# Kernel tuning notes

Hardware: AMD Instinct MI355X
Metric: run time of the kernel (lower is better)

The kernel has to match this reference:

```python
import jax, jax.numpy as jnp
import numpy as np

N_NODES = 50000
N_EDGES = 800000
D_IN, D_HID, D_ENC = 256, 128, 64


def setup_inputs() -> dict:
    key = jax.random.key(0)
    ks = jax.random.split(key, 8)
    x = jax.random.normal(ks[0], (N_NODES, D_IN), dtype=jnp.float32)
    edge_index = jax.random.randint(ks[1], (2, N_EDGES), 0, N_NODES, dtype=jnp.int64)
    # GCNConv params: lin weight (no bias) + separate bias, stored as [in, out]
    W1 = jax.random.normal(ks[2], (D_IN, D_HID), dtype=jnp.float32) * (1.0 / np.sqrt(D_IN))
    b1 = jnp.zeros((D_HID,), dtype=jnp.float32)
    W2 = jax.random.normal(ks[3], (D_HID, D_ENC), dtype=jnp.float32) * (1.0 / np.sqrt(D_HID))
    b2 = jnp.zeros((D_ENC,), dtype=jnp.float32)
    Wfc = jax.random.normal(ks[4], (D_ENC, 1), dtype=jnp.float32) * (1.0 / np.sqrt(D_ENC))
    bfc = jnp.zeros((1,), dtype=jnp.float32)
    return {"x": x, "edge_index": edge_index, "W1": W1, "b1": b1,
            "W2": W2, "b2": b2, "Wfc": Wfc, "bfc": bfc}


def gcn_conv(x, W, b, row, col, norm, n_nodes):
    """PyG GCNConv (normalize=True): D^-1/2 (A+I) D^-1/2 X W + b."""
    h = x @ W                                   # [N, out]
    msg = h[row] * norm[:, None]                # [E+N, out] gather + scale
    out = jax.ops.segment_sum(msg, col, num_segments=n_nodes)  # scatter-add
    return out + b


def gcn_norm(edge_index, n_nodes, dtype):
    loop = jnp.arange(n_nodes, dtype=edge_index.dtype)
    row = jnp.concatenate([edge_index[0], loop])  # sources
    col = jnp.concatenate([edge_index[1], loop])  # targets
    deg = jax.ops.segment_sum(jnp.ones_like(col, dtype=dtype), col,
                              num_segments=n_nodes)
    dinv = jnp.where(deg > 0, jax.lax.rsqrt(jnp.maximum(deg, 1e-12)), 0.0)
    norm = dinv[row] * dinv[col]
    return row, col, norm


def reference(x, edge_index, W1, b1, W2, b2, Wfc, bfc):
    n = x.shape[0]
    row, col, norm = gcn_norm(edge_index, n, x.dtype)
    h = gcn_conv(x, W1, b1, row, col, norm, n)
    h = jax.nn.relu(h)
    # dropout p=0 / eval mode: identity
    h = gcn_conv(h, W2, b2, row, col, norm, n)
    out = jax.nn.sigmoid(h @ Wfc + bfc)          # [N, 1]
    return out
```

## Files before the change

### kernel.cpp

```cpp
#include <hip/hip_runtime.h>
#include <hip/hip_bf16.h>
#include <cmath>

#define N_NODES 50000
#define N_EDGES 800000
#define D_IN 256
#define D_HID 128
#define D_ENC 64
#define NBUK 128
#define BSH 9
#define BMSK 511
#define BCAP 16384
#define PBF_EPT 8
#define NPARTB 196
#define NGEMB 782
#define NGEMB_H 391
#define GEMM_H2_ROW0 (NGEMB_H * 64)
#define NCSRB 98

typedef short short8 __attribute__((ext_vector_type(8)));
typedef float floatx4 __attribute__((ext_vector_type(4)));
typedef float floatx8 __attribute__((ext_vector_type(8)));
typedef unsigned short ushort8v __attribute__((ext_vector_type(8)));

static __device__ __forceinline__ unsigned short f2bf(float f) {
    unsigned int u = __float_as_uint(f);
    unsigned int r = (u + 0x7FFFu + ((u >> 16) & 1u)) >> 16;
    return (unsigned short)r;
}
static __device__ __forceinline__ float bf2f(unsigned short u) {
    return __uint_as_float(((unsigned int)u) << 16);
}
static __device__ __forceinline__ floatx8 bf2f8(ushort8v u) {
    floatx8 f;
#pragma unroll
    for (int j = 0; j < 8; ++j) f[j] = bf2f(u[j]);
    return f;
}

static __device__ __forceinline__ void wswz(const float* __restrict__ W,
                                            unsigned short* __restrict__ Wsw,
                                            int t, int K, int N) {
    int KS = K / 32;
    int lane = t & 63;
    int ks   = (t >> 6) % KS;
    int ct   = (t >> 6) / KS;
    int m = lane & 15, quad = lane >> 4;
    int kbase = ks * 32 + quad * 8;
    int col   = ct * 16 + m;
#pragma unroll
    for (int j = 0; j < 8; ++j)
        Wsw[t * 8 + j] = f2bf(W[(size_t)(kbase + j) * N + col]);
}

__global__ __launch_bounds__(256) void prep_k(const float* __restrict__ W1,
                                              const float* __restrict__ W2,
                                              const float* __restrict__ b2,
                                              const float* __restrict__ Wfc,
                                              unsigned short* __restrict__ Wsw1,
                                              float* __restrict__ w2fc,
                                              float* __restrict__ b2fc,
                                              int* __restrict__ bcur) {
    int t = blockIdx.x * 256 + threadIdx.x;
    if (t < 4096) wswz(W1, Wsw1, t, D_IN, D_HID);
    else if (t < 4224) {
        int c = t - 4096;
        float s = 0.0f;
#pragma unroll 8
        for (int j = 0; j < D_ENC; ++j) s += W2[c * D_ENC + j] * Wfc[j];
        w2fc[c] = s;
    } else if (t == 4224) {
        float s = 0.0f;
        for (int j = 0; j < D_ENC; ++j) s += b2[j] * Wfc[j];
        b2fc[0] = s;
    } else if (t >= 4225 && t < 4225 + NBUK) {
        bcur[t - 4225] = 0;
    }
}

static __device__ void part_path(char* dynsm, int bid,
                                 const int* __restrict__ rows,
                                 const int* __restrict__ cols,
                                 int* __restrict__ bcur,
                                 unsigned int* __restrict__ brecs) {
    unsigned int* recs = (unsigned int*)dynsm;
    int* h     = (int*)(dynsm + 16384);
    int* ex    = h + NBUK;
    int* gbase = ex + NBUK;
    int tid = threadIdx.x;
    if (tid < NBUK) h[tid] = 0;
    __syncthreads();
    int e0 = bid * 4096;
    unsigned int myrec[PBF_EPT];
    int myb[PBF_EPT];
#pragma unroll
    for (int j = 0; j < PBF_EPT; ++j) {
        int e = e0 + j * 512 + tid;
        if (e < N_EDGES) {
            int s = __builtin_nontemporal_load(&rows[e]);
            int d = __builtin_nontemporal_load(&cols[e]);
            myrec[j] = ((unsigned int)s << 16) | (unsigned int)d;
            myb[j] = d >> BSH;
            atomicAdd(&h[myb[j]], 1);
        } else myb[j] = -1;
    }
    __syncthreads();
    if (tid < NBUK) {
        int c = h[tid];
        gbase[tid] = tid * BCAP + (c ? atomicAdd(&bcur[tid], c) : 0);
        ex[tid] = c;
    }
    __syncthreads();
    for (int off = 1; off < NBUK; off <<= 1) {
        int v = 0;
        if (tid < NBUK && tid >= off) v = ex[tid - off];
        __syncthreads();
        if (tid < NBUK) ex[tid] += v;
        __syncthreads();
    }
    if (tid < NBUK) { ex[tid] -= h[tid]; h[tid] = 0; }
    __syncthreads();
#pragma unroll
    for (int j = 0; j < PBF_EPT; ++j) {
        if (myb[j] >= 0) {
            int p = ex[myb[j]] + atomicAdd(&h[myb[j]], 1);
            recs[p] = myrec[j];
        }
    }
    __syncthreads();
    int w = tid >> 6, lane = tid & 63;
    for (int b = w; b < NBUK; b += 8) {
        int start = ex[b], cnt = h[b], gb = gbase[b];
        int lim = (b + 1) * BCAP;
        for (int i = lane; i < cnt; i += 64) {
            int gp = gb + i;
            if (gp < lim) brecs[gp] = recs[start + i];
        }
    }
}

static __device__ void csr_path(char* dynsm, int b,
                                const unsigned int* __restrict__ brecs,
                                const int* __restrict__ bcur,
                                int* __restrict__ rowptr,
                                int* __restrict__ rowcnt,
                                unsigned short* __restrict__ srcs,
                                float* __restrict__ dinv) {
    int* s   = (int*)dynsm;
    int* cur = (int*)(dynsm + 2048);
    unsigned short* sl = (unsigned short*)(dynsm + 4096);
    int tid = threadIdx.x;
    int cb = bcur[b]; if (cb > BCAP) cb = BCAP;
    int ebeg = b * BCAP, eend = ebeg + cb;
    s[tid] = 0;
    __syncthreads();
    for (int e = ebeg + tid; e < eend; e += 512)
        atomicAdd(&s[brecs[e] & BMSK], 1);
    __syncthreads();
    int v = s[tid];
    for (int off = 1; off < 512; off <<= 1) {
        int t = (tid >= off) ? s[tid - off] : 0;
        __syncthreads();
        s[tid] += t;
        __syncthreads();
    }
    int excl = s[tid] - v;
    cur[tid] = excl;
    int node = (b << BSH) + tid;
    if (node < N_NODES) {
        rowptr[node] = ebeg + excl;
        rowcnt[node] = v;
        dinv[node] = rsqrtf((float)(v + 1));
    }
    __syncthreads();
    for (int e = ebeg + tid; e < eend; e += 512) {
        unsigned int rec = brecs[e];
        int p = atomicAdd(&cur[rec & BMSK], 1);
        sl[p] = (unsigned short)(rec >> 16);
    }
    __syncthreads();
    int nw = (cb + 1) >> 1;
    unsigned int* s32 = (unsigned int*)(srcs + ebeg);
    const unsigned int* l32 = (const unsigned int*)sl;
    for (int t = tid; t < nw; t += 512) s32[t] = l32[t];
}

static __device__ void gemm_path(char* dynsm, int row0,
                                 const floatx4* __restrict__ X4,
                                 const unsigned short* __restrict__ Wsw,
                                 unsigned short* __restrict__ H) {
    constexpr int KP = D_IN + 8;
    unsigned short* As = (unsigned short*)dynsm;
    int tid = threadIdx.x;
    for (int idx = tid; idx < 64 * 64; idx += 512) {
        int r = idx >> 6, c4 = idx & 63;
        int gr = row0 + r;
        floatx4 v = (gr < N_NODES) ? __builtin_nontemporal_load(&X4[(size_t)gr * 64 + c4])
                                   : (floatx4){0, 0, 0, 0};
        __hip_bfloat162 p0 = __float22bfloat162_rn(float2{v[0], v[1]});
        __hip_bfloat162 p1 = __float22bfloat162_rn(float2{v[2], v[3]});
        uint2 u; u.x = *(unsigned int*)&p0; u.y = *(unsigned int*)&p1;
        *(uint2*)&As[r * KP + c4 * 4] = u;
    }
    __syncthreads();

    int w    = tid >> 6;
    int lane = tid & 63;
    int m    = lane & 15;
    int quad = lane >> 4;
    int rsub = w & 3;
    int cth  = w >> 2;

    floatx4 acc[4];
#pragma unroll
    for (int ct = 0; ct < 4; ++ct)
#pragma unroll
        for (int i = 0; i < 4; ++i) acc[ct][i] = 0.0f;

#pragma unroll
    for (int ks = 0; ks < D_IN / 32; ++ks) {
        short8 af = *(const short8*)&As[(rsub * 16 + m) * KP + ks * 32 + quad * 8];
#pragma unroll
        for (int ct = 0; ct < 4; ++ct) {
            int ct4 = cth * 4 + ct;
            short8 bf = *(const short8*)&Wsw[(size_t)((ct4 * (D_IN / 32) + ks) * 64 + lane) * 8];
            acc[ct] = __builtin_amdgcn_mfma_f32_16x16x32_bf16(af, bf, acc[ct], 0, 0, 0);
        }
    }

    int rbase = row0 + rsub * 16 + quad * 4;
#pragma unroll
    for (int ct = 0; ct < 4; ++ct) {
        int col = (cth * 4 + ct) * 16 + m;
#pragma unroll
        for (int reg = 0; reg < 4; ++reg) {
            int r = rbase + reg;
            if (r < N_NODES) H[(size_t)r * D_HID + col] = f2bf(acc[ct][reg]);
        }
    }
}

__global__ __launch_bounds__(512) void pg1_k(const int* __restrict__ rows,
                                             const int* __restrict__ cols,
                                             int* __restrict__ bcur,
                                             unsigned int* __restrict__ brecs,
                                             const floatx4* __restrict__ X4,
                                             const unsigned short* __restrict__ Wsw,
                                             unsigned short* __restrict__ H) {
    extern __shared__ char dynsm[];
    if (blockIdx.x < NPARTB)
        part_path(dynsm, blockIdx.x, rows, cols, bcur, brecs);
    else
        gemm_path(dynsm, (blockIdx.x - NPARTB) * 64, X4, Wsw, H);
}

__global__ __launch_bounds__(512) void cg2_k(const unsigned int* __restrict__ brecs,
                                             const int* __restrict__ bcur,
                                             int* __restrict__ rowptr,
                                             int* __restrict__ rowcnt,
                                             unsigned short* __restrict__ srcs,
                                             float* __restrict__ dinv,
                                             const floatx4* __restrict__ X4,
                                             const unsigned short* __restrict__ Wsw,
                                             unsigned short* __restrict__ H) {
    extern __shared__ char dynsm[];
    if (blockIdx.x < NCSRB)
        csr_path(dynsm, blockIdx.x, brecs, bcur, rowptr, rowcnt, srcs, dinv);
    else
        gemm_path(dynsm, (blockIdx.x - NCSRB) * 64 + GEMM_H2_ROW0, X4, Wsw, H);
}

#define WGATHER(SP)                                                            \
    {                                                                          \
        const auto* sp_ = (SP);                                                \
        int i = 0;                                                             \
        for (; i + 8 <= cnt; i += 8) {                                         \
            int s0 = sp_[i],     s1 = sp_[i + 1], s2 = sp_[i + 2], s3 = sp_[i + 3]; \
            int s4 = sp_[i + 4], s5 = sp_[i + 5], s6 = sp_[i + 6], s7 = sp_[i + 7]; \
            float w0 = dinv[s0], w1 = dinv[s1], w2 = dinv[s2], w3 = dinv[s3];  \
            float w4 = dinv[s4], w5 = dinv[s5], w6 = dinv[s6], w7 = dinv[s7];  \
            ushort8v v0 = hs[(size_t)s0 * 16 + d8], v1 = hs[(size_t)s1 * 16 + d8]; \
            ushort8v v2 = hs[(size_t)s2 * 16 + d8], v3 = hs[(size_t)s3 * 16 + d8]; \
            ushort8v v4 = hs[(size_t)s4 * 16 + d8], v5 = hs[(size_t)s5 * 16 + d8]; \
            ushort8v v6 = hs[(size_t)s6 * 16 + d8], v7 = hs[(size_t)s7 * 16 + d8]; \
            a0 += bf2f8(v0) * w0; a1 += bf2f8(v1) * w1;                        \
            a2 += bf2f8(v2) * w2; a3 += bf2f8(v3) * w3;                        \
            a0 += bf2f8(v4) * w4; a1 += bf2f8(v5) * w5;                        \
            a2 += bf2f8(v6) * w6; a3 += bf2f8(v7) * w7;                        \
        }                                                                      \
        if (i + 4 <= cnt) {                                                    \
            int s0 = sp_[i], s1 = sp_[i + 1], s2 = sp_[i + 2], s3 = sp_[i + 3]; \
            a0 += bf2f8(hs[(size_t)s0 * 16 + d8]) * dinv[s0];                  \
            a1 += bf2f8(hs[(size_t)s1 * 16 + d8]) * dinv[s1];                  \
            a2 += bf2f8(hs[(size_t)s2 * 16 + d8]) * dinv[s2];                  \
            a3 += bf2f8(hs[(size_t)s3 * 16 + d8]) * dinv[s3];                  \
            i += 4;                                                            \
        }                                                                      \
        for (; i < cnt; ++i) {                                                 \
            int s = sp_[i];                                                    \
            a0 += bf2f8(hs[(size_t)s * 16 + d8]) * dinv[s];                    \
        }                                                                      \
    }

__global__ __launch_bounds__(256) void g1z_k(const ushort8v* __restrict__ hs,
                                             const int* __restrict__ rowptr,
                                             const int* __restrict__ rowcnt,
                                             const unsigned short* __restrict__ srcs,
                                             const float* __restrict__ dinv,
                                             const float4* __restrict__ b1_4,
                                             const float4* __restrict__ w2fc4,
                                             float* __restrict__ z) {
    __shared__ unsigned short sidx[1024];
    __shared__ int sb2[2];
    int tid = threadIdx.x;
    int nodeb = blockIdx.x * 16;
    int ln = tid >> 4;
    int d8 = tid & 15;
    int node = nodeb + ln;
    int beg = rowptr[node];
    int cnt = rowcnt[node];
    if (tid == 0)   sb2[0] = beg;
    if (tid == 240) sb2[1] = beg + cnt;
    ushort8v selfv = hs[(size_t)node * 16 + d8];
    float di = dinv[node];
    __syncthreads();
    int base = sb2[0], total = sb2[1] - base;
    for (int t = tid; t < total && t < 1024; t += 256) sidx[t] = srcs[base + t];
    __syncthreads();

    floatx8 a0 = {0,0,0,0,0,0,0,0}, a1 = a0, a2 = a0, a3 = a0;
    if (total <= 1024) {
        WGATHER(sidx + (beg - base))
    } else {
        WGATHER(srcs + beg)
    }
    floatx8 acc = a0 + a1 + a2 + a3 + bf2f8(selfv) * di;
    float4 bA = b1_4[d8 * 2],  bB = b1_4[d8 * 2 + 1];
    float4 wA = w2fc4[d8 * 2], wB = w2fc4[d8 * 2 + 1];
    float s = fmaxf(di * acc[0] + bA.x, 0.0f) * wA.x
            + fmaxf(di * acc[1] + bA.y, 0.0f) * wA.y
            + fmaxf(di * acc[2] + bA.z, 0.0f) * wA.z
            + fmaxf(di * acc[3] + bA.w, 0.0f) * wA.w
            + fmaxf(di * acc[4] + bB.x, 0.0f) * wB.x
            + fmaxf(di * acc[5] + bB.y, 0.0f) * wB.y
            + fmaxf(di * acc[6] + bB.z, 0.0f) * wB.z
            + fmaxf(di * acc[7] + bB.w, 0.0f) * wB.w;
#pragma unroll
    for (int off = 8; off; off >>= 1) s += __shfl_xor(s, off, 16);
    if (d8 == 0) z[node] = di * s;
}

__global__ __launch_bounds__(256) void gatherz_k(const float* __restrict__ z,
                                                 const int* __restrict__ rowptr,
                                                 const int* __restrict__ rowcnt,
                                                 const unsigned short* __restrict__ srcs,
                                                 const float* __restrict__ dinv,
                                                 const float* __restrict__ b2fc,
                                                 const float* __restrict__ bfc,
                                                 float* __restrict__ out) {
    int v = blockIdx.x * 256 + threadIdx.x;
    if (v >= N_NODES) return;
    int beg = rowptr[v], cnt = rowcnt[v];
    float s0 = z[v], s1 = 0.0f, s2 = 0.0f, s3 = 0.0f;
    int i = beg, end = beg + cnt;
    for (; i + 4 <= end; i += 4) {
        s0 += z[srcs[i]];
        s1 += z[srcs[i + 1]];
        s2 += z[srcs[i + 2]];
        s3 += z[srcs[i + 3]];
    }
    for (; i < end; ++i) s0 += z[srcs[i]];
    float p = dinv[v] * (s0 + s1 + s2 + s3) + b2fc[0] + bfc[0];
    out[v] = 1.0f / (1.0f + expf(-p));
}

extern "C" void kernel_launch(void* const* d_in, const int* in_sizes, int n_in,
                              void* d_out, int out_size, void* d_ws, size_t ws_size,
                              hipStream_t stream) {
    const float* x   = (const float*)d_in[0];
    const int*   ei  = (const int*)d_in[1];
    const float* W1  = (const float*)d_in[2];
    const float* b1  = (const float*)d_in[3];
    const float* W2  = (const float*)d_in[4];
    const float* b2  = (const float*)d_in[5];
    const float* Wfc = (const float*)d_in[6];
    const float* bfc = (const float*)d_in[7];
    float* out = (float*)d_out;

    const int* rows = ei;
    const int* cols = ei + N_EDGES;

    float* ws     = (float*)d_ws;
    float* dinv   = ws;
    int*   rowptr = (int*)(ws + 50048);
    int*   rowcnt = rowptr + 50048;
    int*   bcur   = rowcnt + 50048;
    unsigned int* brecs = (unsigned int*)(bcur + 128);
    unsigned short* srcs = (unsigned short*)(brecs + NBUK * BCAP);
    unsigned short* h1 = srcs + (size_t)NBUK * BCAP;
    unsigned short* Wsw1 = h1 + (size_t)N_NODES * D_HID;
    float* z    = (float*)(Wsw1 + (size_t)D_IN * D_HID);
    float* w2fc = z + 50000;
    float* b2fc = w2fc + 128;

    prep_k<<<18, 256, 0, stream>>>(W1, W2, b2, Wfc, Wsw1, w2fc, b2fc, bcur);

    pg1_k<<<NPARTB + NGEMB_H, 512, 36864, stream>>>(rows, cols, bcur, brecs,
                                                    (const floatx4*)x, Wsw1, h1);

    cg2_k<<<NCSRB + NGEMB_H, 512, 36864, stream>>>(brecs, bcur, rowptr, rowcnt, srcs, dinv,
                                                   (const floatx4*)x, Wsw1, h1);

    g1z_k<<<N_NODES / 16, 256, 0, stream>>>((const ushort8v*)h1, rowptr, rowcnt, srcs, dinv,
                                            (const float4*)b1, (const float4*)w2fc, z);

    gatherz_k<<<(N_NODES + 255) / 256, 256, 0, stream>>>(z, rowptr, rowcnt, srcs, dinv,
                                                         b2fc, bfc, out);
}
```

Before: 162.7 us.

## Fuse CSR build with first-layer gather and compute degrees via global atomics

Partitioning now also counts in-degrees with global atomics, so the whole X·W1 GEMM runs in a single launch together with edge bucketing. The CSR build (now 512 buckets of 128 nodes) is merged into the layer-1 gather kernel. That kernel sorts sources in LDS and aggregates from the local list, computing dinv of each neighbour on the fly from rowcnt. This removes one launch and a round trip through global memory for srcs. The cost is 800k global atomics, duplicated bucket sorting across the two parity blocks per bucket, and extra rsqrt work per edge.

```diff
diff --git a/kernel.cpp b/kernel.cpp
--- a/kernel.cpp
+++ b/kernel.cpp
@@ -7,16 +7,16 @@
 #define D_IN 256
 #define D_HID 128
 #define D_ENC 64
-#define NBUK 128
-#define BSH 9
-#define BMSK 511
-#define BCAP 16384
+#define NBUK 512
+#define BSH 7
+#define BMSK 127
+#define BCAP 4096
 #define PBF_EPT 8
 #define NPARTB 196
 #define NGEMB 782
-#define NGEMB_H 391
-#define GEMM_H2_ROW0 (NGEMB_H * 64)
-#define NCSRB 98
+#define NBUKU 391
+#define NCZB  782
+#define DYN_LDS 36864
 
 typedef short short8 __attribute__((ext_vector_type(8)));
 typedef float floatx4 __attribute__((ext_vector_type(4)));
@@ -60,29 +60,28 @@
                                               unsigned short* __restrict__ Wsw1,
                                               float* __restrict__ w2fc,
                                               float* __restrict__ b2fc,
-                                              int* __restrict__ bcur) {
-    int t = blockIdx.x * 256 + threadIdx.x;
-    if (t < 4096) wswz(W1, Wsw1, t, D_IN, D_HID);
-    else if (t < 4224) {
-        int c = t - 4096;
+                                              int* __restrict__ bcur,
+                                              int* __restrict__ rowcnt) {
+    int gid = blockIdx.x * 256 + threadIdx.x;
+    if (gid < 4096) wswz(W1, Wsw1, gid, D_IN, D_HID);
+    else if (gid < 4224) {
+        int c = gid - 4096;
         float s = 0.0f;
 #pragma unroll 8
         for (int j = 0; j < D_ENC; ++j) s += W2[c * D_ENC + j] * Wfc[j];
         w2fc[c] = s;
-    } else if (t == 4224) {
+    } else if (gid == 4224) {
         float s = 0.0f;
         for (int j = 0; j < D_ENC; ++j) s += b2[j] * Wfc[j];
         b2fc[0] = s;
-    } else if (t >= 4225 && t < 4225 + NBUK) {
-        bcur[t - 4225] = 0;
-    }
+    }
+    if (gid < NBUK) bcur[gid] = 0;
+    for (int i = gid; i < 50048; i += 16384) rowcnt[i] = 0;
 }
 
 static __device__ void part_path(char* dynsm, int bid,
-                                 const int* __restrict__ rows,
-                                 const int* __restrict__ cols,
-                                 int* __restrict__ bcur,
-                                 unsigned int* __restrict__ brecs) {
+                                 const int* rows, const int* cols,
+                                 int* bcur, unsigned int* brecs, int* rowcnt) {
     unsigned int* recs = (unsigned int*)dynsm;
     int* h     = (int*)(dynsm + 16384);
     int* ex    = h + NBUK;
@@ -102,6 +101,7 @@
             myrec[j] = ((unsigned int)s << 16) | (unsigned int)d;
             myb[j] = d >> BSH;
             atomicAdd(&h[myb[j]], 1);
+            atomicAdd(&rowcnt[d], 1);
         } else myb[j] = -1;
     }
     __syncthreads();
@@ -139,56 +139,9 @@
     }
 }
 
-static __device__ void csr_path(char* dynsm, int b,
-                                const unsigned int* __restrict__ brecs,
-                                const int* __restrict__ bcur,
-                                int* __restrict__ rowptr,
-                                int* __restrict__ rowcnt,
-                                unsigned short* __restrict__ srcs,
-                                float* __restrict__ dinv) {
-    int* s   = (int*)dynsm;
-    int* cur = (int*)(dynsm + 2048);
-    unsigned short* sl = (unsigned short*)(dynsm + 4096);
-    int tid = threadIdx.x;
-    int cb = bcur[b]; if (cb > BCAP) cb = BCAP;
-    int ebeg = b * BCAP, eend = ebeg + cb;
-    s[tid] = 0;
-    __syncthreads();
-    for (int e = ebeg + tid; e < eend; e += 512)
-        atomicAdd(&s[brecs[e] & BMSK], 1);
-    __syncthreads();
-    int v = s[tid];
-    for (int off = 1; off < 512; off <<= 1) {
-        int t = (tid >= off) ? s[tid - off] : 0;
-        __syncthreads();
-        s[tid] += t;
-        __syncthreads();
-    }
-    int excl = s[tid] - v;
-    cur[tid] = excl;
-    int node = (b << BSH) + tid;
-    if (node < N_NODES) {
-        rowptr[node] = ebeg + excl;
-        rowcnt[node] = v;
-        dinv[node] = rsqrtf((float)(v + 1));
-    }
-    __syncthreads();
-    for (int e = ebeg + tid; e < eend; e += 512) {
-        unsigned int rec = brecs[e];
-        int p = atomicAdd(&cur[rec & BMSK], 1);
-        sl[p] = (unsigned short)(rec >> 16);
-    }
-    __syncthreads();
-    int nw = (cb + 1) >> 1;
-    unsigned int* s32 = (unsigned int*)(srcs + ebeg);
-    const unsigned int* l32 = (const unsigned int*)sl;
-    for (int t = tid; t < nw; t += 512) s32[t] = l32[t];
-}
-
 static __device__ void gemm_path(char* dynsm, int row0,
-                                 const floatx4* __restrict__ X4,
-                                 const unsigned short* __restrict__ Wsw,
-                                 unsigned short* __restrict__ H) {
+                                 const floatx4* X4, const unsigned short* Wsw,
+                                 unsigned short* H) {
     constexpr int KP = D_IN + 8;
     unsigned short* As = (unsigned short*)dynsm;
     int tid = threadIdx.x;
@@ -240,114 +193,137 @@
     }
 }
 
-__global__ __launch_bounds__(512) void pg1_k(const int* __restrict__ rows,
-                                             const int* __restrict__ cols,
-                                             int* __restrict__ bcur,
-                                             unsigned int* __restrict__ brecs,
-                                             const floatx4* __restrict__ X4,
-                                             const unsigned short* __restrict__ Wsw,
-                                             unsigned short* __restrict__ H) {
+__global__ __launch_bounds__(512) void pg_k(const int* __restrict__ rows,
+                                            const int* __restrict__ cols,
+                                            int* __restrict__ bcur,
+                                            unsigned int* __restrict__ brecs,
+                                            int* __restrict__ rowcnt,
+                                            const floatx4* __restrict__ X4,
+                                            const unsigned short* __restrict__ Wsw,
+                                            unsigned short* __restrict__ H) {
     extern __shared__ char dynsm[];
     if (blockIdx.x < NPARTB)
-        part_path(dynsm, blockIdx.x, rows, cols, bcur, brecs);
+        part_path(dynsm, blockIdx.x, rows, cols, bcur, brecs, rowcnt);
     else
         gemm_path(dynsm, (blockIdx.x - NPARTB) * 64, X4, Wsw, H);
 }
 
-__global__ __launch_bounds__(512) void cg2_k(const unsigned int* __restrict__ brecs,
-                                             const int* __restrict__ bcur,
-                                             int* __restrict__ rowptr,
-                                             int* __restrict__ rowcnt,
-                                             unsigned short* __restrict__ srcs,
-                                             float* __restrict__ dinv,
-                                             const floatx4* __restrict__ X4,
-                                             const unsigned short* __restrict__ Wsw,
-                                             unsigned short* __restrict__ H) {
-    extern __shared__ char dynsm[];
-    if (blockIdx.x < NCSRB)
-        csr_path(dynsm, blockIdx.x, brecs, bcur, rowptr, rowcnt, srcs, dinv);
-    else
-        gemm_path(dynsm, (blockIdx.x - NCSRB) * 64 + GEMM_H2_ROW0, X4, Wsw, H);
-}
-
-#define WGATHER(SP)                                                            \
+#define WGATHER_RC(SP)                                                         \
     {                                                                          \
-        const auto* sp_ = (SP);                                                \
+        const unsigned short* sp_ = (SP);                                      \
         int i = 0;                                                             \
         for (; i + 8 <= cnt; i += 8) {                                         \
             int s0 = sp_[i],     s1 = sp_[i + 1], s2 = sp_[i + 2], s3 = sp_[i + 3]; \
             int s4 = sp_[i + 4], s5 = sp_[i + 5], s6 = sp_[i + 6], s7 = sp_[i + 7]; \
-            float w0 = dinv[s0], w1 = dinv[s1], w2 = dinv[s2], w3 = dinv[s3];  \
-            float w4 = dinv[s4], w5 = dinv[s5], w6 = dinv[s6], w7 = dinv[s7];  \
+            int c0 = rcg[s0], c1 = rcg[s1], c2 = rcg[s2], c3 = rcg[s3];        \
+            int c4 = rcg[s4], c5 = rcg[s5], c6 = rcg[s6], c7 = rcg[s7];        \
             ushort8v v0 = hs[(size_t)s0 * 16 + d8], v1 = hs[(size_t)s1 * 16 + d8]; \
             ushort8v v2 = hs[(size_t)s2 * 16 + d8], v3 = hs[(size_t)s3 * 16 + d8]; \
             ushort8v v4 = hs[(size_t)s4 * 16 + d8], v5 = hs[(size_t)s5 * 16 + d8]; \
             ushort8v v6 = hs[(size_t)s6 * 16 + d8], v7 = hs[(size_t)s7 * 16 + d8]; \
-            a0 += bf2f8(v0) * w0; a1 += bf2f8(v1) * w1;                        \
-            a2 += bf2f8(v2) * w2; a3 += bf2f8(v3) * w3;                        \
-            a0 += bf2f8(v4) * w4; a1 += bf2f8(v5) * w5;                        \
-            a2 += bf2f8(v6) * w6; a3 += bf2f8(v7) * w7;                        \
+            a0 += bf2f8(v0) * rsqrtf((float)(c0 + 1));                         \
+            a1 += bf2f8(v1) * rsqrtf((float)(c1 + 1));                         \
+            a2 += bf2f8(v2) * rsqrtf((float)(c2 + 1));                         \
+            a3 += bf2f8(v3) * rsqrtf((float)(c3 + 1));                         \
+            a0 += bf2f8(v4) * rsqrtf((float)(c4 + 1));                         \
+            a1 += bf2f8(v5) * rsqrtf((float)(c5 + 1));                         \
+            a2 += bf2f8(v6) * rsqrtf((float)(c6 + 1));                         \
+            a3 += bf2f8(v7) * rsqrtf((float)(c7 + 1));                         \
         }                                                                      \
         if (i + 4 <= cnt) {                                                    \
             int s0 = sp_[i], s1 = sp_[i + 1], s2 = sp_[i + 2], s3 = sp_[i + 3]; \
-            a0 += bf2f8(hs[(size_t)s0 * 16 + d8]) * dinv[s0];                  \
-            a1 += bf2f8(hs[(size_t)s1 * 16 + d8]) * dinv[s1];                  \
-            a2 += bf2f8(hs[(size_t)s2 * 16 + d8]) * dinv[s2];                  \
-            a3 += bf2f8(hs[(size_t)s3 * 16 + d8]) * dinv[s3];                  \
+            a0 += bf2f8(hs[(size_t)s0 * 16 + d8]) * rsqrtf((float)(rcg[s0] + 1)); \
+            a1 += bf2f8(hs[(size_t)s1 * 16 + d8]) * rsqrtf((float)(rcg[s1] + 1)); \
+            a2 += bf2f8(hs[(size_t)s2 * 16 + d8]) * rsqrtf((float)(rcg[s2] + 1)); \
+            a3 += bf2f8(hs[(size_t)s3 * 16 + d8]) * rsqrtf((float)(rcg[s3] + 1)); \
             i += 4;                                                            \
         }                                                                      \
         for (; i < cnt; ++i) {                                                 \
             int s = sp_[i];                                                    \
-            a0 += bf2f8(hs[(size_t)s * 16 + d8]) * dinv[s];                    \
+            a0 += bf2f8(hs[(size_t)s * 16 + d8]) * rsqrtf((float)(rcg[s] + 1)); \
         }                                                                      \
     }
 
-__global__ __launch_bounds__(256) void g1z_k(const ushort8v* __restrict__ hs,
-                                             const int* __restrict__ rowptr,
-                                             const int* __restrict__ rowcnt,
-                                             const unsigned short* __restrict__ srcs,
-                                             const float* __restrict__ dinv,
-                                             const float4* __restrict__ b1_4,
-                                             const float4* __restrict__ w2fc4,
-                                             float* __restrict__ z) {
-    __shared__ unsigned short sidx[1024];
-    __shared__ int sb2[2];
+__global__ __launch_bounds__(512) void cz_k(const unsigned int* __restrict__ brecs,
+                                            const int* __restrict__ bcur,
+                                            int* __restrict__ rowptr,
+                                            const int* __restrict__ rowcnt,
+                                            float* __restrict__ dinv,
+                                            unsigned short* __restrict__ srcs,
+                                            const ushort8v* __restrict__ hs,
+                                            const float4* __restrict__ b1_4,
+                                            const float4* __restrict__ w2fc4,
+                                            float* __restrict__ z) {
+    __shared__ int ex[128], cur[128], rc[128];
+    __shared__ unsigned short sl[BCAP];
+    const int* rcg = rowcnt;
     int tid = threadIdx.x;
-    int nodeb = blockIdx.x * 16;
-    int ln = tid >> 4;
-    int d8 = tid & 15;
-    int node = nodeb + ln;
-    int beg = rowptr[node];
-    int cnt = rowcnt[node];
-    if (tid == 0)   sb2[0] = beg;
-    if (tid == 240) sb2[1] = beg + cnt;
-    ushort8v selfv = hs[(size_t)node * 16 + d8];
-    float di = dinv[node];
-    __syncthreads();
-    int base = sb2[0], total = sb2[1] - base;
-    for (int t = tid; t < total && t < 1024; t += 256) sidx[t] = srcs[base + t];
-    __syncthreads();
-
-    floatx8 a0 = {0,0,0,0,0,0,0,0}, a1 = a0, a2 = a0, a3 = a0;
-    if (total <= 1024) {
-        WGATHER(sidx + (beg - base))
-    } else {
-        WGATHER(srcs + beg)
-    }
-    floatx8 acc = a0 + a1 + a2 + a3 + bf2f8(selfv) * di;
-    float4 bA = b1_4[d8 * 2],  bB = b1_4[d8 * 2 + 1];
-    float4 wA = w2fc4[d8 * 2], wB = w2fc4[d8 * 2 + 1];
-    float s = fmaxf(di * acc[0] + bA.x, 0.0f) * wA.x
-            + fmaxf(di * acc[1] + bA.y, 0.0f) * wA.y
-            + fmaxf(di * acc[2] + bA.z, 0.0f) * wA.z
-            + fmaxf(di * acc[3] + bA.w, 0.0f) * wA.w
-            + fmaxf(di * acc[4] + bB.x, 0.0f) * wB.x
-            + fmaxf(di * acc[5] + bB.y, 0.0f) * wB.y
-            + fmaxf(di * acc[6] + bB.z, 0.0f) * wB.z
-            + fmaxf(di * acc[7] + bB.w, 0.0f) * wB.w;
-#pragma unroll
-    for (int off = 8; off; off >>= 1) s += __shfl_xor(s, off, 16);
-    if (d8 == 0) z[node] = di * s;
+    int b = blockIdx.x >> 1, par = blockIdx.x & 1;
+    int cb = bcur[b]; if (cb > BCAP) cb = BCAP;
+    int ebeg = b * BCAP;
+    if (tid < 128) ex[tid] = 0;
+    __syncthreads();
+    for (int e = tid; e < cb; e += 512)
+        atomicAdd(&ex[brecs[ebeg + e] & BMSK], 1);
+    __syncthreads();
+    int v = (tid < 128) ? ex[tid] : 0;
+    for (int off = 1; off < 128; off <<= 1) {
+        int t = (tid < 128 && tid >= off) ? ex[tid - off] : 0;
+        __syncthreads();
+        if (tid < 128) ex[tid] += t;
+        __syncthreads();
+    }
+    if (tid < 128) {
+        int excl = ex[tid] - v;
+        cur[tid] = excl;
+        rc[tid]  = v;
+        ex[tid]  = excl;
+        int node = (b << BSH) + tid;
+        if (par == 0 && node < N_NODES) {
+            rowptr[node] = ebeg + excl;
+            dinv[node]   = rsqrtf((float)(v + 1));
+        }
+    }
+    __syncthreads();
+    for (int e = tid; e < cb; e += 512) {
+        unsigned int rec = brecs[ebeg + e];
+        int p = atomicAdd(&cur[rec & BMSK], 1);
+        sl[p] = (unsigned short)(rec >> 16);
+    }
+    __syncthreads();
+    if (par == 0) {
+        int nw = (cb + 1) >> 1;
+        unsigned int* s32 = (unsigned int*)(srcs + ebeg);
+        const unsigned int* l32 = (const unsigned int*)sl;
+        for (int t = tid; t < nw; t += 512) s32[t] = l32[t];
+    }
+
+    int ln = tid >> 4, d8 = tid & 15;
+#pragma unroll
+    for (int r = 0; r < 2; ++r) {
+        int l = par * 64 + r * 32 + ln;
+        int node = (b << BSH) + l;
+        if (node < N_NODES) {
+            int beg = ex[l], cnt = rc[l];
+            floatx8 a0 = {0,0,0,0,0,0,0,0}, a1 = a0, a2 = a0, a3 = a0;
+            WGATHER_RC(sl + beg)
+            float di = rsqrtf((float)(cnt + 1));
+            floatx8 acc = a0 + a1 + a2 + a3 + bf2f8(hs[(size_t)node * 16 + d8]) * di;
+            float4 bA = b1_4[d8 * 2],  bB = b1_4[d8 * 2 + 1];
+            float4 wA = w2fc4[d8 * 2], wB = w2fc4[d8 * 2 + 1];
+            float s = fmaxf(di * acc[0] + bA.x, 0.0f) * wA.x
+                    + fmaxf(di * acc[1] + bA.y, 0.0f) * wA.y
+                    + fmaxf(di * acc[2] + bA.z, 0.0f) * wA.z
+                    + fmaxf(di * acc[3] + bA.w, 0.0f) * wA.w
+                    + fmaxf(di * acc[4] + bB.x, 0.0f) * wB.x
+                    + fmaxf(di * acc[5] + bB.y, 0.0f) * wB.y
+                    + fmaxf(di * acc[6] + bB.z, 0.0f) * wB.z
+                    + fmaxf(di * acc[7] + bB.w, 0.0f) * wB.w;
+#pragma unroll
+            for (int off = 8; off; off >>= 1) s += __shfl_xor(s, off, 16);
+            if (d8 == 0) z[node] = di * s;
+        }
+    }
 }
 
 __global__ __launch_bounds__(256) void gatherz_k(const float* __restrict__ z,
@@ -395,24 +371,22 @@
     int*   rowptr = (int*)(ws + 50048);
     int*   rowcnt = rowptr + 50048;
     int*   bcur   = rowcnt + 50048;
-    unsigned int* brecs = (unsigned int*)(bcur + 128);
-    unsigned short* srcs = (unsigned short*)(brecs + NBUK * BCAP);
+    unsigned int* brecs = (unsigned int*)(bcur + 512);
+    unsigned short* srcs = (unsigned short*)(brecs + (size_t)NBUK * BCAP);
     unsigned short* h1 = srcs + (size_t)NBUK * BCAP;
     unsigned short* Wsw1 = h1 + (size_t)N_NODES * D_HID;
     float* z    = (float*)(Wsw1 + (size_t)D_IN * D_HID);
     float* w2fc = z + 50000;
     float* b2fc = w2fc + 128;
 
-    prep_k<<<18, 256, 0, stream>>>(W1, W2, b2, Wfc, Wsw1, w2fc, b2fc, bcur);
-
-    pg1_k<<<NPARTB + NGEMB_H, 512, 36864, stream>>>(rows, cols, bcur, brecs,
-                                                    (const floatx4*)x, Wsw1, h1);
-
-    cg2_k<<<NCSRB + NGEMB_H, 512, 36864, stream>>>(brecs, bcur, rowptr, rowcnt, srcs, dinv,
+    prep_k<<<64, 256, 0, stream>>>(W1, W2, b2, Wfc, Wsw1, w2fc, b2fc, bcur, rowcnt);
+
+    pg_k<<<NPARTB + NGEMB, 512, DYN_LDS, stream>>>(rows, cols, bcur, brecs, rowcnt,
                                                    (const floatx4*)x, Wsw1, h1);
 
-    g1z_k<<<N_NODES / 16, 256, 0, stream>>>((const ushort8v*)h1, rowptr, rowcnt, srcs, dinv,
-                                            (const float4*)b1, (const float4*)w2fc, z);
+    cz_k<<<NCZB, 512, 0, stream>>>(brecs, bcur, rowptr, rowcnt, dinv, srcs,
+                                   (const ushort8v*)h1, (const float4*)b1,
+                                   (const float4*)w2fc, z);
 
     gatherz_k<<<(N_NODES + 255) / 256, 256, 0, stream>>>(z, rowptr, rowcnt, srcs, dinv,
                                                          b2fc, bfc, out);
```

Result: slower. 197.1 us (+21.1%).
